# Performance work log

Hardware: AMD Instinct MI355X
Metric: run time of the kernel (lower is better)

The kernel has to match this reference:

```python
import jax, jax.numpy as jnp
import numpy as np

IN_F = 4096
OUT_F = 4096
TOKENS = 8192


def _ternarize(w):
    # scale = 1 / max(mean|w|, 1e-5); quantize to {-1,0,1} then dequantize
    scale = 1.0 / jnp.maximum(jnp.mean(jnp.abs(w)), 1e-5)
    q = jnp.clip(jnp.round(w * scale), -1.0, 1.0)
    return q / scale


def setup_inputs() -> dict:
    key = jax.random.key(0)
    k1, k2, k3, k4 = jax.random.split(key, 4)
    std = np.sqrt(1.0 / IN_F).astype(np.float32)
    return {
        "quant_x_re": jax.random.normal(k1, (TOKENS, IN_F), dtype=jnp.float32),
        "quant_x_im": jax.random.normal(k2, (TOKENS, IN_F), dtype=jnp.float32),
        "weight_re": jax.random.normal(k3, (OUT_F, IN_F), dtype=jnp.float32) * std,
        "weight_im": jax.random.normal(k4, (OUT_F, IN_F), dtype=jnp.float32) * std,
    }


def reference(quant_x_re, quant_x_im, weight_re, weight_im):
    # STE: forward uses dequantized ternary weights, gradient passes to full-precision w
    w_re = weight_re + jax.lax.stop_gradient(_ternarize(weight_re) - weight_re)
    w_im = weight_im + jax.lax.stop_gradient(_ternarize(weight_im) - weight_im)
    # complex matmul via 4 real GEMMs: y = x @ w^T (complex)
    y_re = quant_x_re @ w_re.T - quant_x_im @ w_im.T
    y_im = quant_x_re @ w_im.T + quant_x_im @ w_re.T
    return (y_re, y_im)
```

## Files before the change

### kernel.cpp

```cpp
#include <hip/hip_runtime.h>
#include <hip/hip_bf16.h>
#include <stdint.h>

#define MDIM 8192
#define NHALF 4096
#define KHALF 4096
#define KDIM 8192
#define OUT_HALF ((size_t)MDIM * NHALF)
#define NT 64
#define SFIX (127.0f / 6.0f)

typedef int i32x4 __attribute__((ext_vector_type(4)));

static __device__ __forceinline__ void glds16(const uint8_t* g, uint8_t* l) {
  __builtin_amdgcn_global_load_lds(
      (const __attribute__((address_space(1))) uint32_t*)g,
      (__attribute__((address_space(3))) uint32_t*)l, 16, 0, 0);
}

__global__ void abssum_partials(const float* __restrict__ wre,
                                const float* __restrict__ wim,
                                float* __restrict__ partials) {
  const int b = blockIdx.x;
  const float4* w4 = (const float4*)((b < 1024) ? wre : wim);
  const int bb = b & 1023;
  float s = 0.f;
  for (int i = bb * 256 + threadIdx.x; i < 4194304; i += 262144) {
    float4 v = w4[i];
    s += fabsf(v.x) + fabsf(v.y) + fabsf(v.z) + fabsf(v.w);
  }
  __shared__ float red[256];
  red[threadIdx.x] = s;
  __syncthreads();
  for (int off = 128; off > 0; off >>= 1) {
    if (threadIdx.x < off) red[threadIdx.x] += red[threadIdx.x + off];
    __syncthreads();
  }
  if (threadIdx.x == 0) partials[b] = red[0];
}

__global__ void finalize_scales(const float* __restrict__ partials,
                                float* __restrict__ sc) {
  __shared__ double red[512];
  const int tid = threadIdx.x;
  double s = 0.0, si = 0.0;
  for (int i = tid; i < 1024; i += 256) s += (double)partials[i];
  for (int i = tid; i < 1024; i += 256) si += (double)partials[1024 + i];
  red[tid] = s;
  red[256 + tid] = si;
  __syncthreads();
  for (int off = 128; off > 0; off >>= 1) {
    if (tid < off) {
      red[tid] += red[tid + off];
      red[256 + tid] += red[256 + tid + off];
    }
    __syncthreads();
  }
  if (tid == 0) {
    const float are = fmaxf((float)(red[0] * (1.0 / 16777216.0)), 1e-5f);
    const float aim = fmaxf((float)(red[256] * (1.0 / 16777216.0)), 1e-5f);
    sc[0] = are;
    sc[1] = aim;
    sc[4] = are / SFIX;
    sc[5] = aim / SFIX;
  }
}

static __device__ __forceinline__ uint32_t q8b(float x, float s) {
  return (uint32_t)((int)fminf(fmaxf(rintf(x * s), -127.f), 127.f)) & 0xffu;
}
static __device__ __forceinline__ uint32_t pack4(float4 v, float s) {
  return q8b(v.x, s) | (q8b(v.y, s) << 8) | (q8b(v.z, s) << 16) | (q8b(v.w, s) << 24);
}
static __device__ __forceinline__ uint32_t q8t(float x, float inv, float sg) {
  return (uint32_t)((int)(fminf(fmaxf(rintf(x * inv), -1.f), 1.f) * sg)) & 0xffu;
}
static __device__ __forceinline__ uint32_t pack4t(float4 v, float inv, float sg) {
  return q8t(v.x, inv, sg) | (q8t(v.y, inv, sg) << 8) |
         (q8t(v.z, inv, sg) << 16) | (q8t(v.w, inv, sg) << 24);
}

__global__ void pack_AB_i8(const float* __restrict__ xre,
                           const float* __restrict__ xim,
                           const float* __restrict__ wre,
                           const float* __restrict__ wim,
                           const float* __restrict__ sc,
                           uint8_t* __restrict__ A, uint8_t* __restrict__ B) {
  const int b = blockIdx.x;
  if (b < 4096) {
    const int t = b * 256 + threadIdx.x;
    const int n = t >> 8;
    const int j = t & 255;
    const float ire = 1.0f / sc[0], iim = 1.0f / sc[1];
    const float4* sre = (const float4*)(wre + (size_t)n * KHALF + j * 16);
    const float4* sim = (const float4*)(wim + (size_t)n * KHALF + j * 16);
    const float4 r0 = sre[0], r1 = sre[1], r2 = sre[2], r3 = sre[3];
    const float4 i0 = sim[0], i1 = sim[1], i2 = sim[2], i3 = sim[3];
    uint4 qre, qimn, qimp;
    qre.x = pack4t(r0, ire, 1.f); qre.y = pack4t(r1, ire, 1.f);
    qre.z = pack4t(r2, ire, 1.f); qre.w = pack4t(r3, ire, 1.f);
    qimn.x = pack4t(i0, iim, -1.f); qimn.y = pack4t(i1, iim, -1.f);
    qimn.z = pack4t(i2, iim, -1.f); qimn.w = pack4t(i3, iim, -1.f);
    qimp.x = pack4t(i0, iim, 1.f); qimp.y = pack4t(i1, iim, 1.f);
    qimp.z = pack4t(i2, iim, 1.f); qimp.w = pack4t(i3, iim, 1.f);
    *(uint4*)(B + (size_t)n * KDIM + j * 16) = qre;
    *(uint4*)(B + (size_t)n * KDIM + KHALF + j * 16) = qimn;
    *(uint4*)(B + (size_t)(n + 4096) * KDIM + j * 16) = qimp;
    *(uint4*)(B + (size_t)(n + 4096) * KDIM + KHALF + j * 16) = qre;
  } else {
    const int t = (b - 4096) * 256 + threadIdx.x;
    const int m = t >> 9;
    const int cc = t & 511;
    const float* src = ((cc < 256) ? xre : xim) + (size_t)m * KHALF + (cc & 255) * 16;
    const float4* s4 = (const float4*)src;
    uint4 o;
    o.x = pack4(s4[0], SFIX); o.y = pack4(s4[1], SFIX);
    o.z = pack4(s4[2], SFIX); o.w = pack4(s4[3], SFIX);
    *(uint4*)(A + (size_t)m * KDIM + cc * 16) = o;
  }
}

__global__ __launch_bounds__(512, 1) void gemm256_i8(
    const uint8_t* __restrict__ A, const uint8_t* __restrict__ B,
    const float* __restrict__ sc, float* __restrict__ out) {
  extern __shared__ uint8_t smem[];

  const int tid = threadIdx.x;
  const int lane = tid & 63;
  const int wave = tid >> 6;
  const int wr = wave >> 2;
  const int wc = wave & 3;
  const int llo = lane & 15, lhi = lane >> 4;

  const int wg = (blockIdx.x & 7) * 128 + (blockIdx.x >> 3);
  const int by = wg & 31;
  const int bx = wg >> 5;

  const int lam = tid >> 3;
  const int u = (tid & 7) ^ (lam & 7);
  const int grow = 2 * lam + (u >> 2);
  const int gcolb = (u & 3) * 16;
  const uint8_t* gA0 = A + (size_t)(by * 256 + grow) * KDIM + gcolb;
  const uint8_t* gA1 = gA0 + (size_t)128 * KDIM;
  const uint8_t* gB0 = B + (size_t)(bx * 256 + grow) * KDIM + gcolb;
  const uint8_t* gB1 = gB0 + (size_t)128 * KDIM;

  i32x4 acc[8][4];
#pragma unroll
  for (int i = 0; i < 8; ++i)
#pragma unroll
    for (int j = 0; j < 4; ++j) acc[i][j] = (i32x4){0, 0, 0, 0};

  const int pslot = (((llo & 1) << 2) + lhi) ^ ((llo >> 1) & 7);
  const int aoff = (wr * 64 + (llo >> 1)) * 128 + pslot * 16;
  const int boff = (wc * 32 + (llo >> 1)) * 128 + pslot * 16;

#define STAGE(T, KH, BUFOFF)                                                  \
  {                                                                           \
    const uint32_t ko = (uint32_t)(T) * 128 + (KH) * 64;                      \
    glds16(gA0 + ko, smem + (BUFOFF) + (KH) * 16384 + tid * 16);              \
    glds16(gA1 + ko, smem + (BUFOFF) + (KH) * 16384 + 8192 + tid * 16);       \
    glds16(gB0 + ko, smem + (BUFOFF) + 32768 + (KH) * 16384 + tid * 16);      \
    glds16(gB1 + ko, smem + (BUFOFF) + 32768 + (KH) * 16384 + 8192 + tid * 16); \
  }

#define VMC(N) asm volatile("s_waitcnt vmcnt(" #N ")" ::: "memory")

#define PHASE_COMPUTE(KH, CB)                                                 \
  {                                                                           \
    const uint8_t* Abase = smem + (CB) + (KH) * 16384 + aoff;                 \
    const uint8_t* Bbase = smem + (CB) + 32768 + (KH) * 16384 + boff;         \
    i32x4 av[8], bv[4];                                                       \
    _Pragma("unroll") for (int i = 0; i < 8; ++i)                             \
        av[i] = *(const i32x4*)(Abase + i * 1024);                            \
    _Pragma("unroll") for (int j = 0; j < 4; ++j)                             \
        bv[j] = *(const i32x4*)(Bbase + j * 1024);                            \
    __builtin_amdgcn_s_setprio(1);                                            \
    _Pragma("unroll") for (int i = 0; i < 8; ++i)                             \
    _Pragma("unroll") for (int j = 0; j < 4; ++j)                             \
        acc[i][j] = __builtin_amdgcn_mfma_i32_16x16x64_i8(av[i], bv[j],       \
                                                          acc[i][j], 0, 0, 0);\
    __builtin_amdgcn_s_setprio(0);                                            \
  }

  STAGE(0, 0, 0)
  STAGE(0, 1, 0)

  for (int t = 0; t < NT - 1; ++t) {
    const uint32_t cb = (uint32_t)(t & 1) << 16;
    const uint32_t sb = cb ^ 65536;

    VMC(4);
    __builtin_amdgcn_s_barrier();
    __builtin_amdgcn_sched_barrier(0);
    STAGE(t + 1, 0, sb)
    PHASE_COMPUTE(0, cb)

    VMC(4);
    __builtin_amdgcn_s_barrier();
    __builtin_amdgcn_sched_barrier(0);
    STAGE(t + 1, 1, sb)
    PHASE_COMPUTE(1, cb)
  }

  {
    const uint32_t cb = (uint32_t)((NT - 1) & 1) << 16;
    VMC(4);
    __builtin_amdgcn_s_barrier();
    __builtin_amdgcn_sched_barrier(0);
    PHASE_COMPUTE(0, cb)
    VMC(0);
    __builtin_amdgcn_s_barrier();
    __builtin_amdgcn_sched_barrier(0);
    PHASE_COMPUTE(1, cb)
  }
#undef STAGE
#undef VMC
#undef PHASE_COMPUTE

  const float fac = (bx < 16) ? sc[4] : sc[5];
  const int mbase = by * 256 + wr * 128 + lhi * 4;
  const int nbase = bx * 256 + wc * 64 + llo;
  float* Cbase = (bx < 16) ? out : (out + OUT_HALF - NHALF);
#pragma unroll
  for (int i = 0; i < 8; ++i)
#pragma unroll
    for (int j = 0; j < 4; ++j) {
      const int n = nbase + j * 16;
#pragma unroll
      for (int r = 0; r < 4; ++r) {
        const int m = mbase + i * 16 + r;
        Cbase[(size_t)m * NHALF + n] = (float)acc[i][j][r] * fac;
      }
    }
}

extern "C" void kernel_launch(void* const* d_in, const int* in_sizes, int n_in,
                              void* d_out, int out_size, void* d_ws, size_t ws_size,
                              hipStream_t stream) {
  const float* xre = (const float*)d_in[0];
  const float* xim = (const float*)d_in[1];
  const float* wre = (const float*)d_in[2];
  const float* wim = (const float*)d_in[3];
  float* out = (float*)d_out;

  uint8_t* A = (uint8_t*)d_ws;
  uint8_t* B = A + (size_t)67108864;
  float* partials = (float*)((uint8_t*)d_ws + (size_t)134217728);
  float* scales = partials + 2048;

  (void)hipFuncSetAttribute((const void*)gemm256_i8,
                            hipFuncAttributeMaxDynamicSharedMemorySize, 131072);

  hipLaunchKernelGGL(abssum_partials, dim3(2048), dim3(256), 0, stream, wre, wim, partials);
  hipLaunchKernelGGL(finalize_scales, dim3(1), dim3(256), 0, stream, partials, scales);
  hipLaunchKernelGGL(pack_AB_i8, dim3(20480), dim3(256), 0, stream, xre, xim, wre, wim, scales, A, B);
  hipLaunchKernelGGL(gemm256_i8, dim3(1024), dim3(512), 131072, stream, A, B, scales, out);
}
```

Measured before the change: 691.3 us.

## Deepen LDS pipeline to four-phase ring and prefetch A fragments into registers

Replaces the double-buffered two-half-tile loop with a four-slot ring of 32KB LDS phases, keeping three global-to-LDS loads in flight. A fragments for the next phase are read from LDS into alternating register sets while the current phase's MFMAs run, so LDS read latency overlaps with matrix math. In exchange it uses more registers for the second A set, which could lower occupancy or cause spills, and the barrier placement relies on the ring slot not being overwritten while it is still being read.

```diff
diff --git a/kernel.cpp b/kernel.cpp
--- a/kernel.cpp
+++ b/kernel.cpp
@@ -155,68 +155,101 @@
   const int aoff = (wr * 64 + (llo >> 1)) * 128 + pslot * 16;
   const int boff = (wc * 32 + (llo >> 1)) * 128 + pslot * 16;
 
-#define STAGE(T, KH, BUFOFF)                                                  \
+#define STAGE_P(PP)                                                           \
   {                                                                           \
-    const uint32_t ko = (uint32_t)(T) * 128 + (KH) * 64;                      \
-    glds16(gA0 + ko, smem + (BUFOFF) + (KH) * 16384 + tid * 16);              \
-    glds16(gA1 + ko, smem + (BUFOFF) + (KH) * 16384 + 8192 + tid * 16);       \
-    glds16(gB0 + ko, smem + (BUFOFF) + 32768 + (KH) * 16384 + tid * 16);      \
-    glds16(gB1 + ko, smem + (BUFOFF) + 32768 + (KH) * 16384 + 8192 + tid * 16); \
-  }
+    const uint32_t ko = (uint32_t)((PP) >> 1) * 128 + ((uint32_t)(PP) & 1) * 64; \
+    uint8_t* dst = smem + ((uint32_t)(PP) & 3) * 32768;                       \
+    glds16(gA0 + ko, dst + tid * 16);                                         \
+    glds16(gA1 + ko, dst + 8192 + tid * 16);                                  \
+    glds16(gB0 + ko, dst + 16384 + tid * 16);                                 \
+    glds16(gB1 + ko, dst + 24576 + tid * 16);                                 \
+  }
+
+#define READ_A(SET, PP)                                                       \
+  {                                                                           \
+    const uint8_t* Ab = smem + ((uint32_t)(PP) & 3) * 32768 + aoff;           \
+    _Pragma("unroll") for (int i = 0; i < 8; ++i)                             \
+        SET[i] = *(const i32x4*)(Ab + i * 1024);                              \
+  }
+
+#define READ_B(PP)                                                            \
+  {                                                                           \
+    const uint8_t* Bb = smem + ((uint32_t)(PP) & 3) * 32768 + 16384 + boff;   \
+    _Pragma("unroll") for (int j = 0; j < 4; ++j)                             \
+        bcur[j] = *(const i32x4*)(Bb + j * 1024);                             \
+  }
+
+#define MFMA_P(SET)                                                           \
+  __builtin_amdgcn_s_setprio(1);                                              \
+  _Pragma("unroll") for (int i = 0; i < 8; ++i)                               \
+  _Pragma("unroll") for (int j = 0; j < 4; ++j)                               \
+      acc[i][j] = __builtin_amdgcn_mfma_i32_16x16x64_i8(SET[i], bcur[j],      \
+                                                        acc[i][j], 0, 0, 0);  \
+  __builtin_amdgcn_s_setprio(0);
 
 #define VMC(N) asm volatile("s_waitcnt vmcnt(" #N ")" ::: "memory")
-
-#define PHASE_COMPUTE(KH, CB)                                                 \
-  {                                                                           \
-    const uint8_t* Abase = smem + (CB) + (KH) * 16384 + aoff;                 \
-    const uint8_t* Bbase = smem + (CB) + 32768 + (KH) * 16384 + boff;         \
-    i32x4 av[8], bv[4];                                                       \
-    _Pragma("unroll") for (int i = 0; i < 8; ++i)                             \
-        av[i] = *(const i32x4*)(Abase + i * 1024);                            \
-    _Pragma("unroll") for (int j = 0; j < 4; ++j)                             \
-        bv[j] = *(const i32x4*)(Bbase + j * 1024);                            \
-    __builtin_amdgcn_s_setprio(1);                                            \
-    _Pragma("unroll") for (int i = 0; i < 8; ++i)                             \
-    _Pragma("unroll") for (int j = 0; j < 4; ++j)                             \
-        acc[i][j] = __builtin_amdgcn_mfma_i32_16x16x64_i8(av[i], bv[j],       \
-                                                          acc[i][j], 0, 0, 0);\
-    __builtin_amdgcn_s_setprio(0);                                            \
-  }
-
-  STAGE(0, 0, 0)
-  STAGE(0, 1, 0)
-
-  for (int t = 0; t < NT - 1; ++t) {
-    const uint32_t cb = (uint32_t)(t & 1) << 16;
-    const uint32_t sb = cb ^ 65536;
-
+#define BAR()                      \
+  __builtin_amdgcn_s_barrier();    \
+  __builtin_amdgcn_sched_barrier(0);
+
+  i32x4 r0a[8], r1a[8], bcur[4];
+
+  STAGE_P(0)
+  STAGE_P(1)
+  STAGE_P(2)
+  VMC(8);
+  BAR()
+  READ_A(r0a, 0)
+
+  for (int p = 0; p < 124; p += 2) {
     VMC(4);
-    __builtin_amdgcn_s_barrier();
+    BAR()
+    STAGE_P(p + 3)
+    READ_B(p)
+    READ_A(r1a, p + 1)
     __builtin_amdgcn_sched_barrier(0);
-    STAGE(t + 1, 0, sb)
-    PHASE_COMPUTE(0, cb)
+    MFMA_P(r0a)
 
     VMC(4);
-    __builtin_amdgcn_s_barrier();
+    BAR()
+    STAGE_P(p + 4)
+    READ_B(p + 1)
+    READ_A(r0a, p + 2)
     __builtin_amdgcn_sched_barrier(0);
-    STAGE(t + 1, 1, sb)
-    PHASE_COMPUTE(1, cb)
-  }
-
-  {
-    const uint32_t cb = (uint32_t)((NT - 1) & 1) << 16;
-    VMC(4);
-    __builtin_amdgcn_s_barrier();
-    __builtin_amdgcn_sched_barrier(0);
-    PHASE_COMPUTE(0, cb)
-    VMC(0);
-    __builtin_amdgcn_s_barrier();
-    __builtin_amdgcn_sched_barrier(0);
-    PHASE_COMPUTE(1, cb)
-  }
-#undef STAGE
+    MFMA_P(r1a)
+  }
+
+  VMC(4);
+  BAR()
+  STAGE_P(127)
+  READ_B(124)
+  READ_A(r1a, 125)
+  __builtin_amdgcn_sched_barrier(0);
+  MFMA_P(r0a)
+
+  VMC(4);
+  BAR()
+  READ_B(125)
+  READ_A(r0a, 126)
+  __builtin_amdgcn_sched_barrier(0);
+  MFMA_P(r1a)
+
+  VMC(0);
+  BAR()
+  READ_B(126)
+  READ_A(r1a, 127)
+  __builtin_amdgcn_sched_barrier(0);
+  MFMA_P(r0a)
+
+  READ_B(127)
+  MFMA_P(r1a)
+
+#undef STAGE_P
+#undef READ_A
+#undef READ_B
+#undef MFMA_P
 #undef VMC
-#undef PHASE_COMPUTE
+#undef BAR
 
   const float fac = (bx < 16) ? sc[4] : sc[5];
   const int mbase = by * 256 + wr * 128 + lhi * 4;
```

After: 693.5 us. About the same (+0.3%).
